# Optimization experiments

Measured on AMD Instinct MI355X. Metric: run time of the kernel, lower is better.

## Reference

```python
import jax, jax.numpy as jnp
import numpy as np

V, E, S, NCLASS = 50000, 512, 1024, 2
B, L = 64, 256


def setup_inputs() -> dict:
    key = jax.random.key(0)
    ks = jax.random.split(key, 8)
    inputs = jax.random.randint(ks[0], (B, L), 0, V)
    emb_table = jax.random.normal(ks[1], (V, E), dtype=jnp.float32) * 0.02
    Wc = jax.random.normal(ks[2], (S, 2 * E), dtype=jnp.float32) * (1.0 / np.sqrt(2 * E))
    bc = jnp.zeros((S,), dtype=jnp.float32)
    W1 = jax.random.normal(ks[3], (50, S), dtype=jnp.float32) * (1.0 / np.sqrt(S))
    b1 = jnp.zeros((50,), dtype=jnp.float32)
    W2 = jax.random.normal(ks[4], (NCLASS, 50), dtype=jnp.float32) * (1.0 / np.sqrt(50))
    b2 = jnp.zeros((NCLASS,), dtype=jnp.float32)
    return {"inputs": inputs, "emb_table": emb_table, "Wc": Wc, "bc": bc,
            "W1": W1, "b1": b1, "W2": W2, "b2": b2}


def reference(inputs, emb_table, Wc, bc, W1, b1, W2, b2):
    # [B, L, E] embedding lookup
    w_embs = emb_table[inputs]
    # sliding-window pair concat: [B, L-1, 2E]
    pairs = jnp.concatenate([w_embs[:, :-1, :], w_embs[:, 1:, :]], axis=-1)
    # conv linear: [B, L-1, S]
    conv = jnp.einsum('blf,sf->bls', pairs, Wc) + bc
    # max-pool over positions then sigmoid: [B, S]
    sent = jax.nn.sigmoid(jnp.max(conv, axis=1))
    # classifier: S -> 50 -> NCLASS
    h = jnp.einsum('bs,hs->bh', sent, W1) + b1
    logits = jnp.einsum('bh,ch->bc', h, W2) + b2
    out = jax.nn.log_softmax(logits, axis=1)
    return jnp.squeeze(out, axis=1) if out.shape[1] == 1 else out
```

## Files before the change

### kernel.cpp

```cpp
#include <hip/hip_runtime.h>

#define VV 50000
#define EE 512
#define SS 1024
#define BB 64
#define LL 256
#define NTOK (BB*LL)
#define XROWS_PAD (NTOK + 8)

typedef __attribute__((ext_vector_type(8))) __bf16 bf16x8;
typedef __attribute__((ext_vector_type(4))) float f32x4;
typedef __attribute__((ext_vector_type(4))) unsigned short us4;

static __device__ __forceinline__ unsigned short f2bf(float f) {
    unsigned int u = __float_as_uint(f);
    u += 0x7FFFu + ((u >> 16) & 1u);
    return (unsigned short)(u >> 16);
}

static __device__ __forceinline__ void glds16(const void* g, void* l) {
    __builtin_amdgcn_global_load_lds(
        (const __attribute__((address_space(1))) unsigned int*)g,
        (__attribute__((address_space(3))) unsigned int*)l,
        16, 0, 0);
}

__global__ void gather_bf16_kernel(const int* __restrict__ inputs,
                                   const float* __restrict__ emb,
                                   unsigned short* __restrict__ Xbf) {
    const int t = blockIdx.x;
    const int idx = inputs[t];
    const int tid = threadIdx.x;
    const float4 v = *(const float4*)(emb + (size_t)idx * EE + tid * 4);
    us4 o;
    o.x = f2bf(v.x); o.y = f2bf(v.y); o.z = f2bf(v.z); o.w = f2bf(v.w);
    *(us4*)(Xbf + (size_t)t * EE + tid * 4) = o;
}

__global__ void wc_bf16_kernel(const float* __restrict__ Wc,
                               unsigned short* __restrict__ Wbf,
                               unsigned int* __restrict__ pre) {
    const int i = (blockIdx.x * 256 + threadIdx.x) * 4;
    const float4 v = *(const float4*)(Wc + i);
    us4 o;
    o.x = f2bf(v.x); o.y = f2bf(v.y); o.z = f2bf(v.z); o.w = f2bf(v.w);
    *(us4*)(Wbf + i) = o;
    if (blockIdx.x < BB) {
        uint4 z = {0u, 0u, 0u, 0u};
        *(uint4*)(pre + blockIdx.x * SS + threadIdx.x * 4) = z;
    }
}

__global__ __launch_bounds__(256, 3)
void conv_gemm_kernel(const unsigned short* __restrict__ Xbf,
                      const unsigned short* __restrict__ Wbf,
                      unsigned int* __restrict__ pre) {
    __shared__ unsigned short sX[136 * 64];
    __shared__ unsigned short sW[256 * 64];

    const int tid = threadIdx.x;
    const int w = tid >> 6;
    const int lane = tid & 63;
    const int wx = w & 1;
    const int wy = w >> 1;
    const int m0 = blockIdx.y * 128;
    const int s0 = blockIdx.x * 128;

    f32x4 acc[4][4];
    #pragma unroll
    for (int mt = 0; mt < 4; ++mt)
        #pragma unroll
        for (int nt = 0; nt < 4; ++nt)
            acc[mt][nt] = (f32x4){0.f, 0.f, 0.f, 0.f};

    const int lrow = lane >> 3;
    const int lcolsw = (((lane & 7) ^ lrow) * 8);
    const int quad = lane >> 4;
    const int l15 = lane & 15;
    const int swA  = l15 & 7;
    const int swA1 = (l15 + 1) & 7;

    for (int kt = 0; kt < 8; ++kt) {
        const int k0 = kt * 64;
        #pragma unroll
        for (int i = 0; i < 4; ++i) {
            const int c = w + 4 * i;
            glds16(Xbf + (size_t)(m0 + c * 8 + lrow) * EE + k0 + lcolsw,
                   (char*)sX + c * 1024);
        }
        if (w == 0) {
            glds16(Xbf + (size_t)(m0 + 128 + lrow) * EE + k0 + lcolsw,
                   (char*)sX + 16 * 1024);
        }
        #pragma unroll
        for (int i = 0; i < 8; ++i) {
            const int c = w + 4 * i;
            const int wrow = c * 8 + lrow;
            const int h = wrow >> 7, sl = wrow & 127;
            glds16(Wbf + (size_t)(s0 + sl) * 1024 + h * 512 + k0 + lcolsw,
                   (char*)sW + c * 1024);
        }
        __syncthreads();

        #pragma unroll
        for (int ks = 0; ks < 64; ks += 32) {
            const int cb = (ks >> 3) + quad;
            const int mrb = wy * 64 + l15;
            const int nrb = wx * 64 + l15;
            bf16x8 aA[4], aB[4];
            #pragma unroll
            for (int mt = 0; mt < 4; ++mt) {
                aA[mt] = *(const bf16x8*)(sX + (mrb + mt * 16) * 64 + ((cb ^ swA) << 3));
                aB[mt] = *(const bf16x8*)(sX + (mrb + 1 + mt * 16) * 64 + ((cb ^ swA1) << 3));
            }
            #pragma unroll
            for (int nt = 0; nt < 4; ++nt) {
                const bf16x8 b1f = *(const bf16x8*)(sW + (nrb + nt * 16) * 64 + ((cb ^ swA) << 3));
                const bf16x8 b2f = *(const bf16x8*)(sW + (128 + nrb + nt * 16) * 64 + ((cb ^ swA) << 3));
                #pragma unroll
                for (int mt = 0; mt < 4; ++mt) {
                    acc[mt][nt] = __builtin_amdgcn_mfma_f32_16x16x32_bf16(
                        aA[mt], b1f, acc[mt][nt], 0, 0, 0);
                    acc[mt][nt] = __builtin_amdgcn_mfma_f32_16x16x32_bf16(
                        aB[mt], b2f, acc[mt][nt], 0, 0, 0);
                }
            }
        }
        __syncthreads();
    }

    const int b = m0 >> 8;
    float* smax = (float*)sX;
    #pragma unroll
    for (int nt = 0; nt < 4; ++nt) {
        float cmax = -3.4e38f;
        #pragma unroll
        for (int mt = 0; mt < 4; ++mt) {
            const int rbase = m0 + wy * 64 + mt * 16 + quad * 4;
            #pragma unroll
            for (int r = 0; r < 4; ++r) {
                const float v = acc[mt][nt][r];
                const bool valid = (((rbase + r) & 255) != 255);
                cmax = valid ? fmaxf(cmax, v) : cmax;
            }
        }
        cmax = fmaxf(cmax, __shfl_xor(cmax, 16));
        cmax = fmaxf(cmax, __shfl_xor(cmax, 32));
        if (lane < 16) smax[wy * 128 + wx * 64 + nt * 16 + lane] = cmax;
    }
    __syncthreads();
    if (tid < 128) {
        const float m = fmaxf(smax[tid], smax[128 + tid]);
        const unsigned int u = __float_as_uint(m);
        const unsigned int e = (u & 0x80000000u) ? ~u : (u | 0x80000000u);
        atomicMax(pre + b * SS + s0 + tid, e);
    }
}

__global__ __launch_bounds__(1024)
void classifier_kernel(const unsigned int* __restrict__ pre,
                       const float* __restrict__ bc,
                       const float* __restrict__ W1,
                       const float* __restrict__ b1,
                       const float* __restrict__ W2,
                       const float* __restrict__ b2,
                       float* __restrict__ out) {
    __shared__ float ssig[SS];
    __shared__ float sh[64];
    const int b = blockIdx.x;
    const int tid = threadIdx.x;
    {
        const unsigned int e = pre[b * SS + tid];
        const unsigned int u = (e & 0x80000000u) ? (e & 0x7FFFFFFFu) : ~e;
        const float x = __uint_as_float(u) + bc[tid];
        ssig[tid] = 1.0f / (1.0f + __expf(-x));
    }
    if (tid >= 50 && tid < 64) sh[tid] = 0.f;
    __syncthreads();
    const int w = tid >> 6, lane = tid & 63;
    const float4* sp = (const float4*)ssig;
    for (int j = w; j < 50; j += 16) {
        const float4* wp = (const float4*)(W1 + j * SS);
        float p = 0.f;
        #pragma unroll
        for (int i = 0; i < 4; ++i) {
            const float4 a = sp[lane + i * 64];
            const float4 g = wp[lane + i * 64];
            p += a.x * g.x + a.y * g.y + a.z * g.z + a.w * g.w;
        }
        #pragma unroll
        for (int off = 32; off; off >>= 1) p += __shfl_xor(p, off);
        if (lane == 0) sh[j] = p + b1[j];
    }
    __syncthreads();
    if (w == 0) {
        const float hj = (lane < 50) ? sh[lane] : 0.f;
        const float w2a = (lane < 50) ? W2[lane] : 0.f;
        const float w2b = (lane < 50) ? W2[50 + lane] : 0.f;
        float l0 = hj * w2a, l1 = hj * w2b;
        #pragma unroll
        for (int off = 32; off; off >>= 1) {
            l0 += __shfl_xor(l0, off);
            l1 += __shfl_xor(l1, off);
        }
        if (lane == 0) {
            l0 += b2[0]; l1 += b2[1];
            const float m = fmaxf(l0, l1);
            const float lse = m + logf(expf(l0 - m) + expf(l1 - m));
            out[b * 2 + 0] = l0 - lse;
            out[b * 2 + 1] = l1 - lse;
        }
    }
}

extern "C" void kernel_launch(void* const* d_in, const int* in_sizes, int n_in,
                              void* d_out, int out_size, void* d_ws, size_t ws_size,
                              hipStream_t stream) {
    const int*   inputs = (const int*)  d_in[0];
    const float* emb    = (const float*)d_in[1];
    const float* Wc     = (const float*)d_in[2];
    const float* bc     = (const float*)d_in[3];
    const float* W1     = (const float*)d_in[4];
    const float* b1     = (const float*)d_in[5];
    const float* W2     = (const float*)d_in[6];
    const float* b2     = (const float*)d_in[7];
    float* out = (float*)d_out;

    unsigned short* Xbf = (unsigned short*)d_ws;
    unsigned short* Wbf = Xbf + (size_t)XROWS_PAD * EE;
    unsigned int*   pre = (unsigned int*)(Wbf + (size_t)SS * 1024);

    gather_bf16_kernel<<<NTOK, 128, 0, stream>>>(inputs, emb, Xbf);
    wc_bf16_kernel<<<1024, 256, 0, stream>>>(Wc, Wbf, pre);
    dim3 grid(SS / 128, NTOK / 128);
    conv_gemm_kernel<<<grid, 256, 0, stream>>>(Xbf, Wbf, pre);
    classifier_kernel<<<BB, 1024, 0, stream>>>(pre, bc, W1, b1, W2, b2, out);
}
```

Before: 199.1 us.

## Switch conv GEMM from bf16 to scaled fp8 MFMA with fp8 staging

```diff
diff --git a/kernel.cpp b/kernel.cpp
--- a/kernel.cpp
+++ b/kernel.cpp
@@ -8,15 +8,11 @@
 #define NTOK (BB*LL)
 #define XROWS_PAD (NTOK + 8)
 
-typedef __attribute__((ext_vector_type(8))) __bf16 bf16x8;
+#define SCALE_A 0x79797979
+#define SCALE_B 0x7A7A7A7A
+
+typedef __attribute__((ext_vector_type(8))) int i32x8;
 typedef __attribute__((ext_vector_type(4))) float f32x4;
-typedef __attribute__((ext_vector_type(4))) unsigned short us4;
-
-static __device__ __forceinline__ unsigned short f2bf(float f) {
-    unsigned int u = __float_as_uint(f);
-    u += 0x7FFFu + ((u >> 16) & 1u);
-    return (unsigned short)(u >> 16);
-}
 
 static __device__ __forceinline__ void glds16(const void* g, void* l) {
     __builtin_amdgcn_global_load_lds(
@@ -25,26 +21,41 @@
         16, 0, 0);
 }
 
-__global__ void gather_bf16_kernel(const int* __restrict__ inputs,
-                                   const float* __restrict__ emb,
-                                   unsigned short* __restrict__ Xbf) {
+static __device__ __forceinline__ uint2 pack8_fp8(float4 v0, float4 v1, float s) {
+    int r0 = __builtin_amdgcn_cvt_pk_fp8_f32(v0.x * s, v0.y * s, 0, 0);
+    r0 = __builtin_amdgcn_cvt_pk_fp8_f32(v0.z * s, v0.w * s, r0, 1);
+    int r1 = __builtin_amdgcn_cvt_pk_fp8_f32(v1.x * s, v1.y * s, 0, 0);
+    r1 = __builtin_amdgcn_cvt_pk_fp8_f32(v1.z * s, v1.w * s, r1, 1);
+    uint2 o; o.x = (unsigned)r0; o.y = (unsigned)r1; return o;
+}
+
+static __device__ __forceinline__ i32x8 ldfrag(const unsigned char* rowbase, int c0, int c1) {
+    const uint4 lo = *(const uint4*)(rowbase + c0 * 16);
+    const uint4 hi = *(const uint4*)(rowbase + c1 * 16);
+    i32x8 f;
+    f[0] = lo.x; f[1] = lo.y; f[2] = lo.z; f[3] = lo.w;
+    f[4] = hi.x; f[5] = hi.y; f[6] = hi.z; f[7] = hi.w;
+    return f;
+}
+
+__global__ void gather_fp8_kernel(const int* __restrict__ inputs,
+                                  const float* __restrict__ emb,
+                                  unsigned char* __restrict__ Xq) {
     const int t = blockIdx.x;
     const int idx = inputs[t];
-    const int tid = threadIdx.x;
-    const float4 v = *(const float4*)(emb + (size_t)idx * EE + tid * 4);
-    us4 o;
-    o.x = f2bf(v.x); o.y = f2bf(v.y); o.z = f2bf(v.z); o.w = f2bf(v.w);
-    *(us4*)(Xbf + (size_t)t * EE + tid * 4) = o;
-}
-
-__global__ void wc_bf16_kernel(const float* __restrict__ Wc,
-                               unsigned short* __restrict__ Wbf,
-                               unsigned int* __restrict__ pre) {
-    const int i = (blockIdx.x * 256 + threadIdx.x) * 4;
-    const float4 v = *(const float4*)(Wc + i);
-    us4 o;
-    o.x = f2bf(v.x); o.y = f2bf(v.y); o.z = f2bf(v.z); o.w = f2bf(v.w);
-    *(us4*)(Wbf + i) = o;
+    const int lane = threadIdx.x;
+    const float4 v0 = *(const float4*)(emb + (size_t)idx * EE + lane * 8);
+    const float4 v1 = *(const float4*)(emb + (size_t)idx * EE + lane * 8 + 4);
+    *(uint2*)(Xq + (size_t)t * EE + lane * 8) = pack8_fp8(v0, v1, 64.0f);
+}
+
+__global__ void wc_fp8_kernel(const float* __restrict__ Wc,
+                              unsigned char* __restrict__ Wq,
+                              unsigned int* __restrict__ pre) {
+    const int i = (blockIdx.x * 256 + threadIdx.x) * 8;
+    const float4 v0 = *(const float4*)(Wc + i);
+    const float4 v1 = *(const float4*)(Wc + i + 4);
+    *(uint2*)(Wq + i) = pack8_fp8(v0, v1, 32.0f);
     if (blockIdx.x < BB) {
         uint4 z = {0u, 0u, 0u, 0u};
         *(uint4*)(pre + blockIdx.x * SS + threadIdx.x * 4) = z;
@@ -52,11 +63,11 @@
 }
 
 __global__ __launch_bounds__(256, 3)
-void conv_gemm_kernel(const unsigned short* __restrict__ Xbf,
-                      const unsigned short* __restrict__ Wbf,
+void conv_gemm_kernel(const unsigned char* __restrict__ Xq,
+                      const unsigned char* __restrict__ Wq,
                       unsigned int* __restrict__ pre) {
-    __shared__ unsigned short sX[136 * 64];
-    __shared__ unsigned short sW[256 * 64];
+    __shared__ unsigned char sX[136 * 128];
+    __shared__ unsigned char sW[256 * 128];
 
     const int tid = threadIdx.x;
     const int w = tid >> 6;
@@ -74,22 +85,23 @@
             acc[mt][nt] = (f32x4){0.f, 0.f, 0.f, 0.f};
 
     const int lrow = lane >> 3;
-    const int lcolsw = (((lane & 7) ^ lrow) * 8);
+    const int lcolsw = (((lane & 7) ^ lrow) * 16);
     const int quad = lane >> 4;
     const int l15 = lane & 15;
     const int swA  = l15 & 7;
     const int swA1 = (l15 + 1) & 7;
-
-    for (int kt = 0; kt < 8; ++kt) {
-        const int k0 = kt * 64;
+    const int cb0 = 2 * quad;
+
+    for (int kt = 0; kt < 4; ++kt) {
+        const int k0 = kt * 128;
         #pragma unroll
         for (int i = 0; i < 4; ++i) {
             const int c = w + 4 * i;
-            glds16(Xbf + (size_t)(m0 + c * 8 + lrow) * EE + k0 + lcolsw,
+            glds16(Xq + (size_t)(m0 + c * 8 + lrow) * EE + k0 + lcolsw,
                    (char*)sX + c * 1024);
         }
         if (w == 0) {
-            glds16(Xbf + (size_t)(m0 + 128 + lrow) * EE + k0 + lcolsw,
+            glds16(Xq + (size_t)(m0 + 128 + lrow) * EE + k0 + lcolsw,
                    (char*)sX + 16 * 1024);
         }
         #pragma unroll
@@ -97,32 +109,32 @@
             const int c = w + 4 * i;
             const int wrow = c * 8 + lrow;
             const int h = wrow >> 7, sl = wrow & 127;
-            glds16(Wbf + (size_t)(s0 + sl) * 1024 + h * 512 + k0 + lcolsw,
+            glds16(Wq + (size_t)(s0 + sl) * 1024 + h * 512 + k0 + lcolsw,
                    (char*)sW + c * 1024);
         }
         __syncthreads();
 
         #pragma unroll
-        for (int ks = 0; ks < 64; ks += 32) {
-            const int cb = (ks >> 3) + quad;
-            const int mrb = wy * 64 + l15;
-            const int nrb = wx * 64 + l15;
-            bf16x8 aA[4], aB[4];
+        for (int mg = 0; mg < 2; ++mg) {
+            i32x8 aA[2], aB[2];
             #pragma unroll
-            for (int mt = 0; mt < 4; ++mt) {
-                aA[mt] = *(const bf16x8*)(sX + (mrb + mt * 16) * 64 + ((cb ^ swA) << 3));
-                aB[mt] = *(const bf16x8*)(sX + (mrb + 1 + mt * 16) * 64 + ((cb ^ swA1) << 3));
+            for (int j = 0; j < 2; ++j) {
+                const int r = wy * 64 + (mg * 2 + j) * 16 + l15;
+                aA[j] = ldfrag(sX + r * 128, cb0 ^ swA, (cb0 + 1) ^ swA);
+                aB[j] = ldfrag(sX + (r + 1) * 128, cb0 ^ swA1, (cb0 + 1) ^ swA1);
             }
             #pragma unroll
             for (int nt = 0; nt < 4; ++nt) {
-                const bf16x8 b1f = *(const bf16x8*)(sW + (nrb + nt * 16) * 64 + ((cb ^ swA) << 3));
-                const bf16x8 b2f = *(const bf16x8*)(sW + (128 + nrb + nt * 16) * 64 + ((cb ^ swA) << 3));
+                const int rB = wx * 64 + nt * 16 + l15;
+                const i32x8 b1 = ldfrag(sW + rB * 128, cb0 ^ swA, (cb0 + 1) ^ swA);
+                const i32x8 b2 = ldfrag(sW + (128 + rB) * 128, cb0 ^ swA, (cb0 + 1) ^ swA);
                 #pragma unroll
-                for (int mt = 0; mt < 4; ++mt) {
-                    acc[mt][nt] = __builtin_amdgcn_mfma_f32_16x16x32_bf16(
-                        aA[mt], b1f, acc[mt][nt], 0, 0, 0);
-                    acc[mt][nt] = __builtin_amdgcn_mfma_f32_16x16x32_bf16(
-                        aB[mt], b2f, acc[mt][nt], 0, 0, 0);
+                for (int j = 0; j < 2; ++j) {
+                    const int mt = mg * 2 + j;
+                    acc[mt][nt] = __builtin_amdgcn_mfma_scale_f32_16x16x128_f8f6f4(
+                        aA[j], b1, acc[mt][nt], 0, 0, 0, SCALE_A, 0, SCALE_B);
+                    acc[mt][nt] = __builtin_amdgcn_mfma_scale_f32_16x16x128_f8f6f4(
+                        aB[j], b2, acc[mt][nt], 0, 0, 0, SCALE_A, 0, SCALE_B);
                 }
             }
         }
@@ -226,13 +238,13 @@
     const float* b2     = (const float*)d_in[7];
     float* out = (float*)d_out;
 
-    unsigned short* Xbf = (unsigned short*)d_ws;
-    unsigned short* Wbf = Xbf + (size_t)XROWS_PAD * EE;
-    unsigned int*   pre = (unsigned int*)(Wbf + (size_t)SS * 1024);
-
-    gather_bf16_kernel<<<NTOK, 128, 0, stream>>>(inputs, emb, Xbf);
-    wc_bf16_kernel<<<1024, 256, 0, stream>>>(Wc, Wbf, pre);
+    unsigned char* Xq = (unsigned char*)d_ws;
+    unsigned char* Wq = Xq + (size_t)XROWS_PAD * EE;
+    unsigned int*  pre = (unsigned int*)(Wq + (size_t)SS * 1024);
+
+    gather_fp8_kernel<<<NTOK, 64, 0, stream>>>(inputs, emb, Xq);
+    wc_fp8_kernel<<<512, 256, 0, stream>>>(Wc, Wq, pre);
     dim3 grid(SS / 128, NTOK / 128);
-    conv_gemm_kernel<<<grid, 256, 0, stream>>>(Xbf, Wbf, pre);
+    conv_gemm_kernel<<<grid, 256, 0, stream>>>(Xq, Wq, pre);
     classifier_kernel<<<BB, 1024, 0, stream>>>(pre, bc, W1, b1, W2, b2, out);
 }
```

Result: slower. 207.2 us (+4.0%).
